# Kernel tuning notes

Hardware: AMD Instinct MI355X
Metric: run time of the kernel (lower is better)

Reference implementation:

```python
import jax, jax.numpy as jnp
import numpy as np

N = 50000
E = 800000
D = 64
EPS_BN = 1e-5
EPS_NORM = 1e-12


def _bn_train(x, gamma, beta):
    # BatchNorm1d in training mode: batch stats over axis 0, biased variance
    mu = jnp.mean(x, axis=0, keepdims=True)
    var = jnp.mean((x - mu) ** 2, axis=0, keepdims=True)
    return (x - mu) / jnp.sqrt(var + EPS_BN) * gamma + beta


def setup_inputs() -> dict:
    key = jax.random.key(0)
    ks = jax.random.split(key, 16)
    s = 1.0 / np.sqrt(D)
    s2 = 1.0 / np.sqrt(2 * D)
    return {
        "h": jax.random.normal(ks[0], (N, D), jnp.float32),
        "e": jax.random.normal(ks[1], (E, D), jnp.float32),
        "src": jax.random.randint(ks[2], (E,), 0, N, jnp.int32),
        "dst": jax.random.randint(ks[3], (E,), 0, N, jnp.int32),
        "A_W": jax.random.uniform(ks[4], (D, D), jnp.float32, -s, s),
        "A_b": jax.random.uniform(ks[5], (D,), jnp.float32, -s, s),
        "B_W": jax.random.uniform(ks[6], (D, D), jnp.float32, -s, s),
        "B_b": jax.random.uniform(ks[7], (D,), jnp.float32, -s, s),
        "C_W": jax.random.uniform(ks[8], (D, D), jnp.float32, -s, s),
        "C_b": jax.random.uniform(ks[9], (D,), jnp.float32, -s, s),
        "W_apply": jax.random.uniform(ks[10], (2 * D, D), jnp.float32, -s2, s2),
        "b_apply": jax.random.uniform(ks[11], (D,), jnp.float32, -s2, s2),
        "gamma_h": jnp.ones((D,), jnp.float32),
        "beta_h": jnp.zeros((D,), jnp.float32),
        "gamma_e": jnp.ones((D,), jnp.float32),
        "beta_e": jnp.zeros((D,), jnp.float32),
    }


def reference(h, e, src, dst, A_W, A_b, B_W, B_b, C_W, C_b,
              W_apply, b_apply, gamma_h, beta_h, gamma_e, beta_e):
    h_in, e_in = h, e
    # dropout p=0 -> identity
    Ah = h @ A_W + A_b            # [N, D]
    Bh = h @ B_W + B_b            # [N, D]
    Ce = e @ C_W + C_b            # [E, D]

    # message: e_ij = Ce + Bh_src + Bh_dst ; gated message sigma(e_ij)*Ah_src
    e_ij = Ce + Bh[src] + Bh[dst]                 # [E, D]
    msg = jax.nn.relu(jax.nn.sigmoid(e_ij) * Ah[src])  # [E, D]

    # reduce: per-destination-node max over mailbox
    c = jax.ops.segment_max(msg, dst, num_segments=N)  # [N, D], -inf if empty
    deg = jax.ops.segment_sum(jnp.ones((E,), msg.dtype), dst, num_segments=N)
    c = jnp.where(deg[:, None] > 0, c, 0.0)

    # apply/update: concat -> linear -> L2 normalize -> activation
    bundle = jnp.concatenate([h, c], axis=1) @ W_apply + b_apply  # [N, D]
    norm = jnp.sqrt(jnp.sum(bundle * bundle, axis=1, keepdims=True))
    bundle = bundle / jnp.maximum(norm, EPS_NORM)
    h_new = jax.nn.relu(bundle)

    e_new = jax.nn.relu(e_ij)

    h_new = _bn_train(h_new, gamma_h, beta_h)
    e_new = _bn_train(e_new, gamma_e, beta_e)

    h_out = h_in + h_new
    e_out = e_in + e_new
    return (h_out, e_out)
```

## Files before the change

### kernel.cpp

```cpp
#include <hip/hip_runtime.h>

typedef __attribute__((ext_vector_type(8))) short short8;
typedef __attribute__((ext_vector_type(8))) unsigned short ushort8;
typedef __attribute__((ext_vector_type(4))) float f32x4;
typedef __attribute__((ext_vector_type(4))) unsigned int u32x4;

#define DEV static __device__ __forceinline__

constexpr int NN = 50000;
constexpr int NE = 800000;
constexpr int NT_N = NN / 16;
constexpr int NT_E = NE / 16;
constexpr int NB_SCAN = (NN + 255) / 256;
constexpr float EPS_BN = 1e-5f;
constexpr float EPS_NORM = 1e-12f;

DEV unsigned short f2b(float f) {
  unsigned u = __float_as_uint(f);
  return (unsigned short)((u + 0x7FFFu + ((u >> 16) & 1u)) >> 16);
}
DEV float b2f(unsigned short s) { return __uint_as_float(((unsigned)s) << 16); }

DEV short8 load_a_frag(const float* __restrict__ base, int row, int kbase) {
  const f32x4* p = reinterpret_cast<const f32x4*>(base + row * 64 + kbase);
  f32x4 v0 = p[0], v1 = p[1];
  short8 a;
  a[0] = f2b(v0[0]); a[1] = f2b(v0[1]); a[2] = f2b(v0[2]); a[3] = f2b(v0[3]);
  a[4] = f2b(v1[0]); a[5] = f2b(v1[1]); a[6] = f2b(v1[2]); a[7] = f2b(v1[3]);
  return a;
}

DEV short8 load_w_frag(const float* __restrict__ W, int kbase, int c0, int lane) {
  int kr = kbase + ((lane >> 4) << 3);
  int cc = c0 + (lane & 15);
  short8 b;
#pragma unroll
  for (int j = 0; j < 8; ++j) b[j] = f2b(W[(kr + j) * 64 + cc]);
  return b;
}

DEV f32x4 mfma16(short8 a, short8 b, f32x4 c) {
  return __builtin_amdgcn_mfma_f32_16x16x32_bf16(a, b, c, 0, 0, 0);
}

__global__ void k_init(u32x4* __restrict__ cbuf4, int* __restrict__ deg,
                       float* __restrict__ stats) {
  int i = blockIdx.x * 256 + threadIdx.x;
  u32x4 z = {0u, 0u, 0u, 0u};
  cbuf4[i] = z;
  if (i < NN) deg[i] = 0;
  if (i < 512) stats[i] = 0.0f;
}

__global__ void k_deg(const int* __restrict__ dst, int* __restrict__ deg) {
  int i = blockIdx.x * 256 + threadIdx.x;
  if (i < NE) atomicAdd(&deg[dst[i]], 1);
}

__global__ void k_scan_local(const int* __restrict__ deg, int* __restrict__ off,
                             int* __restrict__ bsum) {
  __shared__ int sh[256];
  int t = threadIdx.x;
  int i = blockIdx.x * 256 + t;
  int v = (i < NN) ? deg[i] : 0;
  sh[t] = v;
  __syncthreads();
  for (int s = 1; s < 256; s <<= 1) {
    int u = (t >= s) ? sh[t - s] : 0;
    __syncthreads();
    sh[t] += u;
    __syncthreads();
  }
  if (i < NN) off[i] = sh[t] - v;
  if (t == 255) bsum[blockIdx.x] = sh[255];
}

__global__ void k_scan_base(const int* __restrict__ bsum, int* __restrict__ bbase) {
  __shared__ int sh[256];
  int t = threadIdx.x;
  int v = (t < NB_SCAN) ? bsum[t] : 0;
  sh[t] = v;
  __syncthreads();
  for (int s = 1; s < 256; s <<= 1) {
    int u = (t >= s) ? sh[t - s] : 0;
    __syncthreads();
    sh[t] += u;
    __syncthreads();
  }
  if (t < NB_SCAN) bbase[t] = sh[t] - v;
}

__global__ void k_scan_fix(const int* __restrict__ bbase, int* __restrict__ off,
                           int* __restrict__ cursor) {
  int i = blockIdx.x * 256 + threadIdx.x;
  if (i < NN) {
    int o = off[i] + bbase[blockIdx.x];
    off[i] = o;
    cursor[i] = o;
  }
}

__global__ void k_scatter(const int* __restrict__ dst, int* __restrict__ cursor,
                          int* __restrict__ perm) {
  int i = blockIdx.x * 256 + threadIdx.x;
  if (i < NE) {
    int p = atomicAdd(&cursor[dst[i]], 1);
    perm[p] = i;
  }
}

__global__ void __launch_bounds__(256) k_node_lin(
    const float* __restrict__ h, const float* __restrict__ AW,
    const float* __restrict__ Ab, const float* __restrict__ BW,
    const float* __restrict__ Bb, float* __restrict__ Ah_p,
    float* __restrict__ Bh_p) {
  int lane = threadIdx.x & 63, warp = threadIdx.x >> 6;
  int tile = blockIdx.x * 4 + warp;
  if (tile >= NT_N) return;
  int r = lane & 15;

  short8 wa[4][2], wb[4][2];
  float ab[4], bb[4];
#pragma unroll
  for (int t = 0; t < 4; ++t) {
#pragma unroll
    for (int kk = 0; kk < 2; ++kk) {
      wa[t][kk] = load_w_frag(AW, kk * 32, t * 16, lane);
      wb[t][kk] = load_w_frag(BW, kk * 32, t * 16, lane);
    }
    ab[t] = Ab[t * 16 + r];
    bb[t] = Bb[t * 16 + r];
  }

  int row0 = tile * 16;
  int ar = row0 + r, kb = (lane >> 4) * 8;
  short8 a0 = load_a_frag(h, ar, kb);
  short8 a1 = load_a_frag(h, ar, 32 + kb);

  f32x4 zero = {0.f, 0.f, 0.f, 0.f};
  f32x4 accA[4], accB[4];
#pragma unroll
  for (int t = 0; t < 4; ++t) {
    accA[t] = mfma16(a0, wa[t][0], zero);
    accA[t] = mfma16(a1, wa[t][1], accA[t]);
    accB[t] = mfma16(a0, wb[t][0], zero);
    accB[t] = mfma16(a1, wb[t][1], accB[t]);
  }
#pragma unroll
  for (int q = 0; q < 4; ++q) {
    int row = row0 + (lane >> 4) * 4 + q;
    f32x4 va = {accA[0][q] + ab[0], accA[1][q] + ab[1], accA[2][q] + ab[2],
                accA[3][q] + ab[3]};
    f32x4 vb = {accB[0][q] + bb[0], accB[1][q] + bb[1], accB[2][q] + bb[2],
                accB[3][q] + bb[3]};
    *reinterpret_cast<f32x4*>(Ah_p + row * 64 + r * 4) = va;
    *reinterpret_cast<f32x4*>(Bh_p + row * 64 + r * 4) = vb;
  }
}

__global__ void __launch_bounds__(256) k_edge_sorted(
    const float* __restrict__ e, const int* __restrict__ src,
    const int* __restrict__ dst, const int* __restrict__ perm,
    const float* __restrict__ CW, const float* __restrict__ Cb,
    const float* __restrict__ Ah_p, const float* __restrict__ Bh_p,
    float* __restrict__ cbuf, unsigned short* __restrict__ stage,
    float* __restrict__ gsum, float* __restrict__ gsq) {
  __shared__ short8 cwL[8][64];
  __shared__ unsigned short mT[4][64][18];
  __shared__ __align__(16) unsigned short eT[4][16][72];
  __shared__ float ssum[64], ssq[64];
  int lane = threadIdx.x & 63, warp = threadIdx.x >> 6;
  int r = lane & 15, hi = lane >> 4;

  for (int j = threadIdx.x; j < 512; j += 256) {
    int t = j >> 7, kk = (j >> 6) & 1, ln = j & 63;
    cwL[t * 2 + kk][ln] = load_w_frag(CW, kk * 32, t * 16, ln);
  }
  float cb4[4];
#pragma unroll
  for (int t = 0; t < 4; ++t) cb4[t] = Cb[t * 16 + r];
  __syncthreads();

  unsigned short (*mTw)[18] = mT[warp];
  unsigned short (*eTw)[72] = eT[warp];

  float es[4] = {0.f, 0.f, 0.f, 0.f}, eq[4] = {0.f, 0.f, 0.f, 0.f};
  f32x4 zero = {0.f, 0.f, 0.f, 0.f};
  int stride = gridDim.x * 4;
  int tile0 = blockIdx.x * 4 + warp;

  int p = 0;
  if (tile0 < NT_E) p = perm[tile0 * 16 + r];

  for (int tile = tile0; tile < NT_E; tile += stride) {
    int tn = tile + stride;
    int p_next = 0, d, s;
    if (tn < NT_E) p_next = perm[tn * 16 + r];
    d = dst[p];
    s = src[p];

    int kb = hi * 8;
    short8 a0 = load_a_frag(e, p, kb);
    short8 a1 = load_a_frag(e, p, 32 + kb);

    f32x4 acc[4];
#pragma unroll
    for (int t = 0; t < 4; ++t) {
      acc[t] = mfma16(a0, cwL[t * 2][lane], zero);
      acc[t] = mfma16(a1, cwL[t * 2 + 1][lane], acc[t]);
    }

#pragma unroll
    for (int q = 0; q < 4; ++q) {
      int rowidx = hi * 4 + q;
      int sq_ = __shfl(s, rowidx);
      int dq_ = __shfl(d, rowidx);
      f32x4 bs = *reinterpret_cast<const f32x4*>(Bh_p + sq_ * 64 + r * 4);
      f32x4 bd = *reinterpret_cast<const f32x4*>(Bh_p + dq_ * 64 + r * 4);
      f32x4 av = *reinterpret_cast<const f32x4*>(Ah_p + sq_ * 64 + r * 4);
#pragma unroll
      for (int t = 0; t < 4; ++t) {
        float eij = acc[t][q] + cb4[t] + bs[t] + bd[t];
        float re = (eij > 0.0f) ? eij : 0.0f;
        es[t] += re;
        eq[t] += re * re;
        eTw[rowidx][t * 16 + r] = f2b(eij);
        float sg = __fdividef(1.0f, 1.0f + __expf(-eij));
        float m = sg * av[t];
        m = (m > 0.0f) ? m : 0.0f;
        mTw[t * 16 + r][rowidx] = f2b(m);
      }
    }
    __builtin_amdgcn_sched_barrier(0);

#pragma unroll
    for (int it = 0; it < 2; ++it) {
      int row = (lane >> 3) + it * 8;
      int seg = lane & 7;
      int er = __shfl(p, row);
      ushort8 v = *reinterpret_cast<const ushort8*>(&eTw[row][seg * 8]);
      *reinterpret_cast<ushort8*>(stage + (size_t)er * 64 + seg * 8) = v;
    }

    unsigned short cur = mTw[lane][0];
    int cur_d = __shfl(d, 0);
    int run_start = 0;
#pragma unroll
    for (int row = 1; row < 16; ++row) {
      unsigned short val = mTw[lane][row];
      int dr = __shfl(d, row);
      if (dr == cur_d) {
        cur = (val > cur) ? val : cur;
      } else {
        float cf = b2f(cur);
        if (run_start == 0)
          atomicMax((unsigned*)&cbuf[cur_d * 64 + lane], __float_as_uint(cf));
        else
          cbuf[cur_d * 64 + lane] = cf;
        cur_d = dr;
        cur = val;
        run_start = row;
      }
    }
    atomicMax((unsigned*)&cbuf[cur_d * 64 + lane], __float_as_uint(b2f(cur)));

    p = p_next;
  }

  if (threadIdx.x < 64) { ssum[threadIdx.x] = 0.f; ssq[threadIdx.x] = 0.f; }
  __syncthreads();
#pragma unroll
  for (int t = 0; t < 4; ++t) {
    int col = t * 16 + r;
    atomicAdd(&ssum[col], es[t]);
    atomicAdd(&ssq[col], eq[t]);
  }
  __syncthreads();
  if (threadIdx.x < 64) {
    atomicAdd(&gsum[threadIdx.x], ssum[threadIdx.x]);
    atomicAdd(&gsq[threadIdx.x], ssq[threadIdx.x]);
  }
}

__global__ void __launch_bounds__(256) k_apply(
    const float* __restrict__ h, float* hc, const float* __restrict__ Wap,
    const float* __restrict__ bap, float* __restrict__ gsum,
    float* __restrict__ gsq) {
  __shared__ float ssum[64], ssq[64];
  int lane = threadIdx.x & 63, warp = threadIdx.x >> 6;
  int tile = blockIdx.x * 4 + warp;
  int r = lane & 15;

  float hs[4] = {0.f, 0.f, 0.f, 0.f}, hq[4] = {0.f, 0.f, 0.f, 0.f};

  if (tile < NT_N) {
    short8 w[4][4];
    float ba[4];
#pragma unroll
    for (int t = 0; t < 4; ++t) {
#pragma unroll
      for (int kk = 0; kk < 4; ++kk) w[t][kk] = load_w_frag(Wap, kk * 32, t * 16, lane);
      ba[t] = bap[t * 16 + r];
    }

    int row0 = tile * 16;
    int ar = row0 + r, kb = (lane >> 4) * 8;
    short8 a0 = load_a_frag(h, ar, kb);
    short8 a1 = load_a_frag(h, ar, 32 + kb);
    short8 a2 = load_a_frag(hc, ar, kb);
    short8 a3 = load_a_frag(hc, ar, 32 + kb);

    f32x4 zero = {0.f, 0.f, 0.f, 0.f};
    f32x4 acc[4];
#pragma unroll
    for (int t = 0; t < 4; ++t) {
      acc[t] = mfma16(a0, w[t][0], zero);
      acc[t] = mfma16(a1, w[t][1], acc[t]);
      acc[t] = mfma16(a2, w[t][2], acc[t]);
      acc[t] = mfma16(a3, w[t][3], acc[t]);
    }

    float v[4][4];
#pragma unroll
    for (int t = 0; t < 4; ++t)
#pragma unroll
      for (int q = 0; q < 4; ++q) v[t][q] = acc[t][q] + ba[t];

#pragma unroll
    for (int q = 0; q < 4; ++q) {
      float sq = v[0][q] * v[0][q] + v[1][q] * v[1][q] + v[2][q] * v[2][q] +
                 v[3][q] * v[3][q];
      sq += __shfl_xor(sq, 1);
      sq += __shfl_xor(sq, 2);
      sq += __shfl_xor(sq, 4);
      sq += __shfl_xor(sq, 8);
      float sc = __fdividef(1.0f, fmaxf(sqrtf(sq), EPS_NORM));
      int row = row0 + (lane >> 4) * 4 + q;
#pragma unroll
      for (int t = 0; t < 4; ++t) {
        float hn = v[t][q] * sc;
        hn = (hn > 0.0f) ? hn : 0.0f;
        hc[row * 64 + t * 16 + r] = hn;
        hs[t] += hn;
        hq[t] += hn * hn;
      }
    }
  }

  if (threadIdx.x < 64) { ssum[threadIdx.x] = 0.f; ssq[threadIdx.x] = 0.f; }
  __syncthreads();
#pragma unroll
  for (int t = 0; t < 4; ++t) {
    int col = t * 16 + r;
    atomicAdd(&ssum[col], hs[t]);
    atomicAdd(&ssq[col], hq[t]);
  }
  __syncthreads();
  if (threadIdx.x < 64) {
    atomicAdd(&gsum[threadIdx.x], ssum[threadIdx.x]);
    atomicAdd(&gsq[threadIdx.x], ssq[threadIdx.x]);
  }
}

__global__ void k_stats(const float* __restrict__ sum_e, const float* __restrict__ sq_e,
                        const float* __restrict__ sum_h, const float* __restrict__ sq_h,
                        const float* __restrict__ gamma_e, const float* __restrict__ beta_e,
                        const float* __restrict__ gamma_h, const float* __restrict__ beta_h,
                        float* __restrict__ se, float* __restrict__ oe,
                        float* __restrict__ sh, float* __restrict__ oh) {
  int j = threadIdx.x;
  if (j < 64) {
    float mu = sum_e[j] / (float)NE;
    float var = fmaxf(sq_e[j] / (float)NE - mu * mu, 0.0f);
    float s = gamma_e[j] / sqrtf(var + EPS_BN);
    se[j] = s;
    oe[j] = beta_e[j] - mu * s;
    mu = sum_h[j] / (float)NN;
    var = fmaxf(sq_h[j] / (float)NN - mu * mu, 0.0f);
    s = gamma_h[j] / sqrtf(var + EPS_BN);
    sh[j] = s;
    oh[j] = beta_h[j] - mu * s;
  }
}

__global__ void __launch_bounds__(256) k_fin_h(const float* __restrict__ h,
                                               const float* __restrict__ sh,
                                               const float* __restrict__ oh,
                                               float* __restrict__ outh) {
  int i = (blockIdx.x * 256 + threadIdx.x) * 4;
  if (i >= NN * 64) return;
  f32x4 x = *reinterpret_cast<const f32x4*>(outh + i);
  f32x4 hv = *reinterpret_cast<const f32x4*>(h + i);
  int c0 = i & 63;
  f32x4 rr;
#pragma unroll
  for (int j = 0; j < 4; ++j) rr[j] = hv[j] + x[j] * sh[c0 + j] + oh[c0 + j];
  *reinterpret_cast<f32x4*>(outh + i) = rr;
}

__global__ void __launch_bounds__(256) k_fin_e_stream(
    const float* __restrict__ e, const unsigned short* __restrict__ stage,
    const float* __restrict__ se, const float* __restrict__ oe,
    float* __restrict__ oute) {
  __shared__ float s_se[64], s_oe[64];
  if (threadIdx.x < 64) {
    s_se[threadIdx.x] = se[threadIdx.x];
    s_oe[threadIdx.x] = oe[threadIdx.x];
  }
  __syncthreads();
  size_t i8 = (size_t)blockIdx.x * 256 + threadIdx.x;
  size_t i = i8 * 8;
  ushort8 sv = *reinterpret_cast<const ushort8*>(stage + i);
  f32x4 e0 = *reinterpret_cast<const f32x4*>(e + i);
  f32x4 e1 = *reinterpret_cast<const f32x4*>(e + i + 4);
  int c0 = (int)(i & 63);
  f32x4 r0, r1;
#pragma unroll
  for (int j = 0; j < 4; ++j) {
    float x = b2f(sv[j]);
    float rx = (x > 0.0f) ? x : 0.0f;
    r0[j] = e0[j] + rx * s_se[c0 + j] + s_oe[c0 + j];
  }
#pragma unroll
  for (int j = 0; j < 4; ++j) {
    float x = b2f(sv[4 + j]);
    float rx = (x > 0.0f) ? x : 0.0f;
    r1[j] = e1[j] + rx * s_se[c0 + 4 + j] + s_oe[c0 + 4 + j];
  }
  *reinterpret_cast<f32x4*>(oute + i) = r0;
  *reinterpret_cast<f32x4*>(oute + i + 4) = r1;
}

extern "C" void kernel_launch(void* const* d_in, const int* in_sizes, int n_in,
                              void* d_out, int out_size, void* d_ws, size_t ws_size,
                              hipStream_t stream) {
  (void)in_sizes; (void)n_in; (void)out_size; (void)ws_size;
  const float* h   = (const float*)d_in[0];
  const float* e   = (const float*)d_in[1];
  const int*   src = (const int*)d_in[2];
  const int*   dst = (const int*)d_in[3];
  const float* AW  = (const float*)d_in[4];
  const float* Ab  = (const float*)d_in[5];
  const float* BW  = (const float*)d_in[6];
  const float* Bb  = (const float*)d_in[7];
  const float* CW  = (const float*)d_in[8];
  const float* Cb  = (const float*)d_in[9];
  const float* Wap = (const float*)d_in[10];
  const float* bap = (const float*)d_in[11];
  const float* gamma_h = (const float*)d_in[12];
  const float* beta_h  = (const float*)d_in[13];
  const float* gamma_e = (const float*)d_in[14];
  const float* beta_e  = (const float*)d_in[15];

  float* ws = (float*)d_ws;
  float* Ah_p  = ws;
  float* Bh_p  = ws + 3200000;
  float* stats = ws + 6400000;
  float* sum_e = stats;
  float* sq_e  = stats + 64;
  float* sum_h = stats + 128;
  float* sq_h  = stats + 192;
  float* se    = stats + 256;
  float* oe    = stats + 320;
  float* sh    = stats + 384;
  float* oh    = stats + 448;

  int* deg    = (int*)(ws + 6400512);
  int* off    = deg + NN;
  int* bsum   = off + NN;
  int* bbase  = bsum + 256;
  int* cursor = bbase + 256;
  int* perm   = cursor + NN;
  unsigned short* stage = (unsigned short*)(ws + 7351024);

  float* outh = (float*)d_out;
  float* oute = outh + (size_t)NN * 64;
  float* cbuf = outh;

  k_init<<<3125, 256, 0, stream>>>((u32x4*)cbuf, deg, stats);
  k_deg<<<(NE + 255) / 256, 256, 0, stream>>>(dst, deg);
  k_scan_local<<<NB_SCAN, 256, 0, stream>>>(deg, off, bsum);
  k_scan_base<<<1, 256, 0, stream>>>(bsum, bbase);
  k_scan_fix<<<NB_SCAN, 256, 0, stream>>>(bbase, off, cursor);
  k_scatter<<<(NE + 255) / 256, 256, 0, stream>>>(dst, cursor, perm);

  k_node_lin<<<(NT_N + 3) / 4, 256, 0, stream>>>(h, AW, Ab, BW, Bb, Ah_p, Bh_p);
  k_edge_sorted<<<2048, 256, 0, stream>>>(e, src, dst, perm, CW, Cb, Ah_p,
                                          Bh_p, cbuf, stage, sum_e, sq_e);
  k_apply<<<(NT_N + 3) / 4, 256, 0, stream>>>(h, cbuf, Wap, bap, sum_h, sq_h);
  k_stats<<<1, 64, 0, stream>>>(sum_e, sq_e, sum_h, sq_h, gamma_e, beta_e,
                                gamma_h, beta_h, se, oe, sh, oh);
  k_fin_h<<<NN * 64 / 1024, 256, 0, stream>>>(h, sh, oh, outh);
  k_fin_e_stream<<<NE * 64 / (256 * 8), 256, 0, stream>>>(e, stage, se, oe, oute);
}
```

Measured before the change: 420.9 us.

## Software-pipeline edge kernel loads and assign contiguous tile ranges per warp

After: 445.7 us. 5.9% more time.

```diff
diff --git a/kernel.cpp b/kernel.cpp
--- a/kernel.cpp
+++ b/kernel.cpp
@@ -21,13 +21,16 @@
 }
 DEV float b2f(unsigned short s) { return __uint_as_float(((unsigned)s) << 16); }
 
-DEV short8 load_a_frag(const float* __restrict__ base, int row, int kbase) {
-  const f32x4* p = reinterpret_cast<const f32x4*>(base + row * 64 + kbase);
-  f32x4 v0 = p[0], v1 = p[1];
+DEV short8 frag_from_f32(f32x4 v0, f32x4 v1) {
   short8 a;
   a[0] = f2b(v0[0]); a[1] = f2b(v0[1]); a[2] = f2b(v0[2]); a[3] = f2b(v0[3]);
   a[4] = f2b(v1[0]); a[5] = f2b(v1[1]); a[6] = f2b(v1[2]); a[7] = f2b(v1[3]);
   return a;
+}
+
+DEV short8 load_a_frag(const float* __restrict__ base, int row, int kbase) {
+  const f32x4* p = reinterpret_cast<const f32x4*>(base + row * 64 + kbase);
+  return frag_from_f32(p[0], p[1]);
 }
 
 DEV short8 load_w_frag(const float* __restrict__ W, int kbase, int c0, int lane) {
@@ -186,38 +189,71 @@
 
   float es[4] = {0.f, 0.f, 0.f, 0.f}, eq[4] = {0.f, 0.f, 0.f, 0.f};
   f32x4 zero = {0.f, 0.f, 0.f, 0.f};
-  int stride = gridDim.x * 4;
-  int tile0 = blockIdx.x * 4 + warp;
-
-  int p = 0;
-  if (tile0 < NT_E) p = perm[tile0 * 16 + r];
-
-  for (int tile = tile0; tile < NT_E; tile += stride) {
-    int tn = tile + stride;
-    int p_next = 0, d, s;
-    if (tn < NT_E) p_next = perm[tn * 16 + r];
-    d = dst[p];
-    s = src[p];
-
-    int kb = hi * 8;
-    short8 a0 = load_a_frag(e, p, kb);
-    short8 a1 = load_a_frag(e, p, 32 + kb);
+  int kb = hi * 8;
+
+  int wid = blockIdx.x * 4 + warp;
+  int nw = gridDim.x * 4;
+  int qn = NT_E / nw, rm = NT_E % nw;
+  int begin = (wid < rm) ? wid * (qn + 1) : rm * (qn + 1) + (wid - rm) * qn;
+  int n = (wid < rm) ? qn + 1 : qn;
+
+  int p_cur = 0, p_nxt = 0, d_cur = 0, s_cur = 0;
+  f32x4 e0c = zero, e1c = zero;
+
+  if (n > 0) {
+    p_cur = perm[begin * 16 + r];
+    d_cur = dst[p_cur];
+    s_cur = src[p_cur];
+    e0c = *reinterpret_cast<const f32x4*>(e + (size_t)p_cur * 64 + kb);
+    e1c = *reinterpret_cast<const f32x4*>(e + (size_t)p_cur * 64 + 32 + kb);
+  }
+  if (n > 1) p_nxt = perm[(begin + 1) * 16 + r];
+
+  for (int i = 0; i < n; ++i) {
+    int p_nn = 0;
+    if (i + 2 < n) p_nn = perm[(begin + i + 2) * 16 + r];
+    int d_n = 0, s_n = 0;
+    f32x4 e0n = zero, e1n = zero;
+    if (i + 1 < n) {
+      d_n = dst[p_nxt];
+      s_n = src[p_nxt];
+      e0n = *reinterpret_cast<const f32x4*>(e + (size_t)p_nxt * 64 + kb);
+      e1n = *reinterpret_cast<const f32x4*>(e + (size_t)p_nxt * 64 + 32 + kb);
+    }
+
+    short8 a0 = frag_from_f32(e0c, e1c) ;
+    (void)a0;
+    f32x4 e0b = *reinterpret_cast<const f32x4*>(e + (size_t)p_cur * 64 + kb + 4);
+    f32x4 e1b = *reinterpret_cast<const f32x4*>(e + (size_t)p_cur * 64 + 36 + kb);
+    short8 af0 = frag_from_f32(e0c, e0b);
+    short8 af1 = frag_from_f32(e1c, e1b);
 
     f32x4 acc[4];
 #pragma unroll
     for (int t = 0; t < 4; ++t) {
-      acc[t] = mfma16(a0, cwL[t * 2][lane], zero);
-      acc[t] = mfma16(a1, cwL[t * 2 + 1][lane], acc[t]);
-    }
-
+      acc[t] = mfma16(af0, cwL[t * 2][lane], zero);
+      acc[t] = mfma16(af1, cwL[t * 2 + 1][lane], acc[t]);
+    }
+
+    int sq4[4], dq4[4];
 #pragma unroll
     for (int q = 0; q < 4; ++q) {
+      sq4[q] = __shfl(s_cur, hi * 4 + q);
+      dq4[q] = __shfl(d_cur, hi * 4 + q);
+    }
+
+    f32x4 bs = *reinterpret_cast<const f32x4*>(Bh_p + (size_t)sq4[0] * 64 + r * 4);
+    f32x4 bd = *reinterpret_cast<const f32x4*>(Bh_p + (size_t)dq4[0] * 64 + r * 4);
+    f32x4 av = *reinterpret_cast<const f32x4*>(Ah_p + (size_t)sq4[0] * 64 + r * 4);
+#pragma unroll
+    for (int q = 0; q < 4; ++q) {
+      f32x4 bs_n = zero, bd_n = zero, av_n = zero;
+      if (q < 3) {
+        bs_n = *reinterpret_cast<const f32x4*>(Bh_p + (size_t)sq4[q + 1] * 64 + r * 4);
+        bd_n = *reinterpret_cast<const f32x4*>(Bh_p + (size_t)dq4[q + 1] * 64 + r * 4);
+        av_n = *reinterpret_cast<const f32x4*>(Ah_p + (size_t)sq4[q + 1] * 64 + r * 4);
+      }
       int rowidx = hi * 4 + q;
-      int sq_ = __shfl(s, rowidx);
-      int dq_ = __shfl(d, rowidx);
-      f32x4 bs = *reinterpret_cast<const f32x4*>(Bh_p + sq_ * 64 + r * 4);
-      f32x4 bd = *reinterpret_cast<const f32x4*>(Bh_p + dq_ * 64 + r * 4);
-      f32x4 av = *reinterpret_cast<const f32x4*>(Ah_p + sq_ * 64 + r * 4);
 #pragma unroll
       for (int t = 0; t < 4; ++t) {
         float eij = acc[t][q] + cb4[t] + bs[t] + bd[t];
@@ -230,6 +266,7 @@
         m = (m > 0.0f) ? m : 0.0f;
         mTw[t * 16 + r][rowidx] = f2b(m);
       }
+      bs = bs_n; bd = bd_n; av = av_n;
     }
     __builtin_amdgcn_sched_barrier(0);
 
@@ -237,18 +274,18 @@
     for (int it = 0; it < 2; ++it) {
       int row = (lane >> 3) + it * 8;
       int seg = lane & 7;
-      int er = __shfl(p, row);
+      int er = __shfl(p_cur, row);
       ushort8 v = *reinterpret_cast<const ushort8*>(&eTw[row][seg * 8]);
       *reinterpret_cast<ushort8*>(stage + (size_t)er * 64 + seg * 8) = v;
     }
 
     unsigned short cur = mTw[lane][0];
-    int cur_d = __shfl(d, 0);
+    int cur_d = __shfl(d_cur, 0);
     int run_start = 0;
 #pragma unroll
     for (int row = 1; row < 16; ++row) {
       unsigned short val = mTw[lane][row];
-      int dr = __shfl(d, row);
+      int dr = __shfl(d_cur, row);
       if (dr == cur_d) {
         cur = (val > cur) ? val : cur;
       } else {
@@ -264,7 +301,9 @@
     }
     atomicMax((unsigned*)&cbuf[cur_d * 64 + lane], __float_as_uint(b2f(cur)));
 
-    p = p_next;
+    p_cur = p_nxt; p_nxt = p_nn;
+    d_cur = d_n; s_cur = s_n;
+    e0c = e0n; e1c = e1n;
   }
 
   if (threadIdx.x < 64) { ssum[threadIdx.x] = 0.f; ssq[threadIdx.x] = 0.f; }
@@ -485,7 +524,7 @@
   k_scatter<<<(NE + 255) / 256, 256, 0, stream>>>(dst, cursor, perm);
 
   k_node_lin<<<(NT_N + 3) / 4, 256, 0, stream>>>(h, AW, Ab, BW, Bb, Ah_p, Bh_p);
-  k_edge_sorted<<<2048, 256, 0, stream>>>(e, src, dst, perm, CW, Cb, Ah_p,
+  k_edge_sorted<<<1024, 256, 0, stream>>>(e, src, dst, perm, CW, Cb, Ah_p,
                                           Bh_p, cbuf, stage, sum_e, sq_e);
   k_apply<<<(NT_N + 3) / 4, 256, 0, stream>>>(h, cbuf, Wap, bap, sum_h, sq_h);
   k_stats<<<1, 64, 0, stream>>>(sum_e, sq_e, sum_h, sq_h, gamma_e, beta_e,
```
